# Performance work log

Measured on AMD Instinct MI355X. Metric: run time of the kernel, lower is better.

Reference implementation:

```python
import jax, jax.numpy as jnp
import numpy as np

N, M, D = 32768, 2048, 32


def setup_inputs() -> dict:
    key = jax.random.key(0)
    k1, k2, k3, k4 = jax.random.split(key, 4)
    inputs = jax.random.normal(k1, (N, D), dtype=jnp.float32)
    # matches torch init: abs(10*randn*0.1 + 0.2)
    gamma = jnp.abs(10.0 * jax.random.normal(k2, (M, D, D), dtype=jnp.float32) * 0.1 + 0.2)
    means = jax.random.normal(k3, (M, D), dtype=jnp.float32)
    weights = jax.random.normal(k4, (M,), dtype=jnp.float32)
    return {"inputs": inputs, "gamma": gamma, "means": means, "weights": weights}


def reference(inputs, gamma, means, weights):
    # cov_m = gamma_m @ gamma_m^T  -> symmetric PSD [M, D, D]
    cov = jnp.einsum('mde,mfe->mdf', gamma, gamma)
    # Quadratic form (x - mu)^T C (x - mu) expanded (C symmetric):
    # x^T C_m x via GEMM on flattened outer products: [N, D*D] @ [D*D, M]
    xx = (inputs[:, :, None] * inputs[:, None, :]).reshape(inputs.shape[0], -1)
    quad_x = xx @ cov.reshape(cov.shape[0], -1).T            # [N, M]
    b = jnp.einsum('mde,me->md', cov, means)                 # C_m mu_m, [M, D]
    cross = inputs @ b.T                                     # x^T C_m mu_m, [N, M]
    const = jnp.einsum('md,md->m', b, means)                 # mu^T C mu, [M]
    D_ij = quad_x - 2.0 * cross + const[None, :]             # [N, M]
    out = jnp.exp(-D_ij) @ weights                           # [N]
    return out[:, None]
```

## Files before the change

### kernel.cpp

```cpp
#include <hip/hip_runtime.h>
#include <math.h>


#define NN 32768
#define MM 2048
#define DDIM 32
#define KSYM 576
#define ROWS 128
#define KSTEPS 18
#define SCREEN 120.0f
#define MCAP 2048
#define FCAP 1000000

typedef __attribute__((ext_vector_type(8))) short short8;
typedef __attribute__((ext_vector_type(4))) float floatx4;

__device__ __forceinline__ unsigned int to_bf16(float f) {
  union { float f; unsigned int u; } x; x.f = f;
  return (x.u + 0x7fffu + ((x.u >> 16) & 1u)) >> 16;
}

struct DFTab { unsigned char d[528]; unsigned char f[528]; };
constexpr DFTab make_df() {
  DFTab t{};
  int s = 0;
  for (int d = 0; d < 32; ++d)
    for (int f = d; f < 32; ++f) {
      t.d[s] = (unsigned char)d; t.f[s] = (unsigned char)f; ++s;
    }
  return t;
}
constexpr DFTab DFT = make_df();

__device__ __forceinline__ float slot_val(const float* v, int s) {
  if (s < 528) return v[DFT.d[s]] * v[DFT.f[s]];
  if (s < 560) return v[s - 528];
  if (s < 562) return 1.f;
  return 0.f;
}

__device__ __forceinline__ void slot_df(int s, int* dd, int* ff) {
  int d = 0, b = 0;
  while (b + (DDIM - d) <= s) { b += DDIM - d; ++d; }
  *dd = d; *ff = d + (s - b);
}

__global__ __launch_bounds__(256) void build_b_kernel(
    const float* __restrict__ gamma, const float* __restrict__ means,
    unsigned short* __restrict__ Bm) {
  __shared__ float G[DDIM][DDIM + 1];
  __shared__ float C[DDIM][DDIM + 1];
  __shared__ float bv[DDIM];
  __shared__ float cc;
  const int m = blockIdx.x;
  const int t = threadIdx.x;
  const float* g = gamma + (size_t)m * DDIM * DDIM;
  for (int l = t; l < DDIM * DDIM; l += 256) G[l >> 5][l & 31] = g[l];
  __syncthreads();
  const float* mu = means + m * DDIM;
  for (int l = t; l < DDIM * DDIM; l += 256) {
    int d = l >> 5, f = l & 31;
    float c = 0.f;
#pragma unroll
    for (int e = 0; e < DDIM; ++e) c += G[d][e] * G[f][e];
    C[d][f] = c;
  }
  __syncthreads();
  if (t < DDIM) {
    float b = 0.f;
#pragma unroll
    for (int f = 0; f < DDIM; ++f) b += C[t][f] * mu[f];
    bv[t] = b;
  }
  __syncthreads();
  if (t == 0) {
    float c = 0.f;
#pragma unroll
    for (int d = 0; d < DDIM; ++d) c += bv[d] * mu[d];
    cc = c;
  }
  __syncthreads();
  unsigned short* brow = Bm + (size_t)m * KSYM;
  for (int s = t; s < KSYM; s += 256) {
    float val;
    if (s < 528) {
      int d, f; slot_df(s, &d, &f);
      val = (d == f) ? C[d][d] : 2.f * C[d][f];
    } else if (s < 560) {
      val = -2.f * bv[s - 528];
    } else if (s == 560) {
      val = cc;
    } else if (s == 561) {
      unsigned int hi = to_bf16(cc);
      union { unsigned int u; float f; } xh; xh.u = hi << 16;
      val = cc - xh.f;
    } else {
      val = 0.f;
    }
    brow[s] = (unsigned short)to_bf16(val);
  }
}

__device__ __noinline__ double survivor_contrib(
    int m, const float* __restrict__ gamma, const float* __restrict__ means,
    const float* __restrict__ weights, const float* __restrict__ xrow) {
  const float* mu = means + m * DDIM;
  float v[DDIM];
#pragma unroll
  for (int d = 0; d < DDIM; ++d) v[d] = xrow[d] - mu[d];
  const float* g = gamma + (size_t)m * DDIM * DDIM;
  float Dex = 0.f;
  for (int e = 0; e < DDIM; ++e) {
    float y = 0.f;
#pragma unroll
    for (int d = 0; d < DDIM; ++d) y += g[d * DDIM + e] * v[d];
    Dex += y * y;
  }
  float e2 = -Dex * 1.44269504088896340736f;
  float kf = floorf(e2);
  float mant = exp2f(e2 - kf);
  return ldexp((double)(weights[m] * mant), (int)kf);
}

__global__ __launch_bounds__(512, 2) void screen_kernel(
    const float* __restrict__ x, const unsigned short* __restrict__ Bm,
    unsigned int* __restrict__ mcnt, unsigned short* __restrict__ mlist,
    unsigned int* __restrict__ flist, unsigned int* __restrict__ fcount) {
  extern __shared__ __align__(16) unsigned short As[];
  const int t = threadIdx.x;
  const int i0 = blockIdx.x * ROWS;
  const int lane = t & 63, w = t >> 6;
  const int lrow = lane & 15, quad = lane >> 4;
  const int rot = blockIdx.x & 31;

  {
    const int r = t >> 2, j = t & 3;
    float v[DDIM];
#pragma unroll
    for (int q = 0; q < 8; ++q)
      *(floatx4*)&v[q * 4] = *(const floatx4*)(x + (size_t)(i0 + r) * DDIM + q * 4);
#pragma unroll
    for (int jj = 0; jj < 4; ++jj) {
      if (j == jj) {
#pragma unroll
        for (int cc = 0; cc < 18; ++cc) {
          const int c = jj * 18 + cc;
          unsigned int uu[4];
#pragma unroll
          for (int q = 0; q < 4; ++q) {
            const int s0 = c * 8 + q * 2;
            uu[q] = to_bf16(slot_val(v, s0)) | (to_bf16(slot_val(v, s0 + 1)) << 16);
          }
          const int cs = (c & ~7) | ((c & 7) ^ (r & 7));
          uint4 o; o.x = uu[0]; o.y = uu[1]; o.z = uu[2]; o.w = uu[3];
          *(uint4*)&As[r * KSYM + cs * 8] = o;
        }
      }
    }
  }
  __syncthreads();

#pragma unroll 1
  for (int g = 0; g < 4; ++g) {
    const int mq = ((g * 8 + w) + rot) & 31;
    const int m0 = mq * 64;
    const unsigned short* bb0 = Bm + (size_t)(m0 +  0 + lrow) * KSYM + quad * 8;
    const unsigned short* bb1 = Bm + (size_t)(m0 + 16 + lrow) * KSYM + quad * 8;
    const unsigned short* bb2 = Bm + (size_t)(m0 + 32 + lrow) * KSYM + quad * 8;
    const unsigned short* bb3 = Bm + (size_t)(m0 + 48 + lrow) * KSYM + quad * 8;

    floatx4 acc[8][4] = {};
#pragma unroll
    for (int kk = 0; kk < KSTEPS; ++kk) {
      short8 bf[4];
      bf[0] = *(const short8*)(bb0 + kk * 32);
      bf[1] = *(const short8*)(bb1 + kk * 32);
      bf[2] = *(const short8*)(bb2 + kk * 32);
      bf[3] = *(const short8*)(bb3 + kk * 32);
      short8 af[8];
#pragma unroll
      for (int ti = 0; ti < 8; ++ti) {
        int rr = ti * 16 + lrow;
        int c = kk * 4 + quad;
        int cs = (c & ~7) | ((c & 7) ^ (rr & 7));
        af[ti] = *(const short8*)&As[rr * KSYM + cs * 8];
      }
#pragma unroll
      for (int ti = 0; ti < 8; ++ti)
#pragma unroll
        for (int mj = 0; mj < 4; ++mj)
          acc[ti][mj] = __builtin_amdgcn_mfma_f32_16x16x32_bf16(
              af[ti], bf[mj], acc[ti][mj], 0, 0, 0);
    }

#pragma unroll
    for (int ti = 0; ti < 8; ++ti)
#pragma unroll
      for (int mj = 0; mj < 4; ++mj)
#pragma unroll
        for (int r = 0; r < 4; ++r) {
          float Dt = acc[ti][mj][r];
          if (Dt < SCREEN) {
            int gi = i0 + ti * 16 + quad * 4 + r;
            int gm = m0 + mj * 16 + lrow;
            unsigned int idx = atomicAdd(&mcnt[gm], 1u);
            if (idx < MCAP) {
              mlist[(size_t)gm * MCAP + idx] = (unsigned short)gi;
            } else {
              unsigned int fi = atomicAdd(fcount, 1u);
              if (fi < FCAP)
                flist[fi] = ((unsigned int)gi << 11) | (unsigned int)gm;
            }
          }
        }
  }
}

__global__ __launch_bounds__(256) void survivor2_kernel(
    const unsigned int* __restrict__ mcnt, const unsigned short* __restrict__ mlist,
    const float* __restrict__ x, const float* __restrict__ gamma,
    const float* __restrict__ means, const float* __restrict__ weights,
    double* __restrict__ acc_out) {
  __shared__ float Gt[DDIM][DDIM + 1];
  __shared__ float mu[DDIM];
  const int m = blockIdx.x;
  const int t = threadIdx.x;
  unsigned int cnt = mcnt[m];
  if (cnt > MCAP) cnt = MCAP;
  if (cnt == 0) return;
  const float* g = gamma + (size_t)m * DDIM * DDIM;
  for (int l = t; l < DDIM * DDIM; l += 256) Gt[l & 31][l >> 5] = g[l];
  if (t < DDIM) mu[t] = means[m * DDIM + t];
  __syncthreads();
  const float wm = weights[m];
  for (unsigned int s = t; s < cnt; s += 256) {
    int gi = mlist[(size_t)m * MCAP + s];
    float v[DDIM];
#pragma unroll
    for (int q = 0; q < 8; ++q) {
      floatx4 xv = *(const floatx4*)(x + (size_t)gi * DDIM + q * 4);
      v[q * 4 + 0] = xv.x - mu[q * 4 + 0];
      v[q * 4 + 1] = xv.y - mu[q * 4 + 1];
      v[q * 4 + 2] = xv.z - mu[q * 4 + 2];
      v[q * 4 + 3] = xv.w - mu[q * 4 + 3];
    }
    float Dex = 0.f;
#pragma unroll
    for (int e = 0; e < DDIM; ++e) {
      float y = 0.f;
#pragma unroll
      for (int d = 0; d < DDIM; ++d) y += Gt[e][d] * v[d];
      Dex += y * y;
    }
    float e2 = -Dex * 1.44269504088896340736f;
    float kf = floorf(e2);
    float mant = exp2f(e2 - kf);
    atomicAdd(&acc_out[gi], ldexp((double)(wm * mant), (int)kf));
  }
}

__global__ __launch_bounds__(256) void survivor_fallback_kernel(
    const unsigned int* __restrict__ flist, const unsigned int* __restrict__ fcount,
    const float* __restrict__ x, const float* __restrict__ gamma,
    const float* __restrict__ means, const float* __restrict__ weights,
    double* __restrict__ acc_out) {
  unsigned int total = *fcount;
  if (total > FCAP) total = FCAP;
  for (unsigned int idx = blockIdx.x * 256 + threadIdx.x; idx < total;
       idx += gridDim.x * 256) {
    unsigned int p = flist[idx];
    int gi = (int)(p >> 11), gm = (int)(p & 2047u);
    double c = survivor_contrib(gm, gamma, means, weights, x + (size_t)gi * DDIM);
    atomicAdd(&acc_out[gi], c);
  }
}

__global__ __launch_bounds__(256) void finalize_kernel(
    const double* __restrict__ acc, float* __restrict__ out) {
  int i = blockIdx.x * 256 + threadIdx.x;
  out[i] = (float)acc[i];
}

extern "C" void kernel_launch(void* const* d_in, const int* in_sizes, int n_in,
                              void* d_out, int out_size, void* d_ws, size_t ws_size,
                              hipStream_t stream) {
  (void)in_sizes; (void)n_in; (void)out_size;
  const float* x       = (const float*)d_in[0];
  const float* gamma   = (const float*)d_in[1];
  const float* means   = (const float*)d_in[2];
  const float* weights = (const float*)d_in[3];

  char* p = (char*)d_ws;
  double* acc          = (double*)p;            p += (size_t)NN * 8;
  unsigned int* fcount = (unsigned int*)p;      p += 16;
  unsigned int* mcnt   = (unsigned int*)p;      p += (size_t)MM * 4;
  unsigned short* mlist= (unsigned short*)p;    p += (size_t)MM * MCAP * 2;
  unsigned int* flist  = (unsigned int*)p;      p += (size_t)FCAP * 4;
  unsigned short* Bm   = (unsigned short*)p;    p += (size_t)MM * KSYM * 2;
  const size_t needed = (size_t)(p - (char*)d_ws);
  const size_t zero_bytes = (size_t)NN * 8 + 16 + (size_t)MM * 4;
  if (ws_size < needed) return;

  (void)hipFuncSetAttribute((const void*)screen_kernel,
                            hipFuncAttributeMaxDynamicSharedMemorySize,
                            ROWS * KSYM * 2);

  hipMemsetAsync(d_ws, 0, zero_bytes, stream);
  hipLaunchKernelGGL(build_b_kernel, dim3(MM), dim3(256), 0, stream, gamma, means, Bm);
  hipLaunchKernelGGL(screen_kernel, dim3(NN / ROWS), dim3(512),
                     ROWS * KSYM * 2, stream,
                     x, Bm, mcnt, mlist, flist, fcount);
  hipLaunchKernelGGL(survivor2_kernel, dim3(MM), dim3(256), 0, stream,
                     mcnt, mlist, x, gamma, means, weights, acc);
  hipLaunchKernelGGL(survivor_fallback_kernel, dim3(256), dim3(256), 0, stream,
                     flist, fcount, x, gamma, means, weights, acc);
  hipLaunchKernelGGL(finalize_kernel, dim3(NN / 256), dim3(256), 0, stream,
                     acc, (float*)d_out);
}
```

Measured before the change: 185.6 us.

## Screen with FP8 scaled MFMA and per-component thresholds, merge fallback kernel

The screening GEMM moves from bf16 16x16x32 MFMA to FP8 16x16x128 scaled MFMA. Each component's coefficient row gets a power-of-two block scale, and the constant term becomes a per-component threshold (SCREEN - c), so K drops from 576 to 640 bytes in 5 steps. The screen margin rises to absorb FP8 error, which may admit more survivors into the exact recomputation. The fallback survivor kernel is folded into the main survivor kernel as extra blocks to save a launch.

```diff
diff --git a/kernel.cpp b/kernel.cpp
--- a/kernel.cpp
+++ b/kernel.cpp
@@ -5,15 +5,16 @@
 #define NN 32768
 #define MM 2048
 #define DDIM 32
-#define KSYM 576
+#define KQ 640
 #define ROWS 128
-#define KSTEPS 18
-#define SCREEN 120.0f
+#define KSTEPS 5
+#define SCREEN 160.0f
 #define MCAP 2048
 #define FCAP 1000000
-
-typedef __attribute__((ext_vector_type(8))) short short8;
+#define FBLK 64
+
 typedef __attribute__((ext_vector_type(4))) float floatx4;
+typedef __attribute__((ext_vector_type(8))) int int8v;
 
 __device__ __forceinline__ unsigned int to_bf16(float f) {
   union { float f; unsigned int u; } x; x.f = f;
@@ -35,7 +36,6 @@
 __device__ __forceinline__ float slot_val(const float* v, int s) {
   if (s < 528) return v[DFT.d[s]] * v[DFT.f[s]];
   if (s < 560) return v[s - 528];
-  if (s < 562) return 1.f;
   return 0.f;
 }
 
@@ -47,11 +47,13 @@
 
 __global__ __launch_bounds__(256) void build_b_kernel(
     const float* __restrict__ gamma, const float* __restrict__ means,
-    unsigned short* __restrict__ Bm) {
+    unsigned char* __restrict__ Bm8, unsigned char* __restrict__ sB,
+    float* __restrict__ th) {
   __shared__ float G[DDIM][DDIM + 1];
   __shared__ float C[DDIM][DDIM + 1];
   __shared__ float bv[DDIM];
   __shared__ float cc;
+  __shared__ float rmax[64];
   const int m = blockIdx.x;
   const int t = threadIdx.x;
   const float* g = gamma + (size_t)m * DDIM * DDIM;
@@ -79,25 +81,56 @@
     for (int d = 0; d < DDIM; ++d) c += bv[d] * mu[d];
     cc = c;
   }
-  __syncthreads();
-  unsigned short* brow = Bm + (size_t)m * KSYM;
-  for (int s = t; s < KSYM; s += 256) {
-    float val;
-    if (s < 528) {
-      int d, f; slot_df(s, &d, &f);
-      val = (d == f) ? C[d][d] : 2.f * C[d][f];
-    } else if (s < 560) {
-      val = -2.f * bv[s - 528];
-    } else if (s == 560) {
-      val = cc;
-    } else if (s == 561) {
-      unsigned int hi = to_bf16(cc);
-      union { unsigned int u; float f; } xh; xh.u = hi << 16;
-      val = cc - xh.f;
-    } else {
-      val = 0.f;
-    }
-    brow[s] = (unsigned short)to_bf16(val);
+  float vals[4];
+  float lmax = 0.f;
+  __syncthreads();
+  if (t < 140) {
+#pragma unroll
+    for (int q = 0; q < 4; ++q) {
+      int s = t * 4 + q;
+      float val;
+      if (s < 528) {
+        int d, f; slot_df(s, &d, &f);
+        val = (d == f) ? C[d][d] : 2.f * C[d][f];
+      } else if (s < 560) {
+        val = -2.f * bv[s - 528];
+      } else {
+        val = 0.f;
+      }
+      vals[q] = val;
+      lmax = fmaxf(lmax, fabsf(val));
+    }
+  }
+  if (t < 64) rmax[t] = 0.f;
+  __syncthreads();
+  if (t < 140) {
+    float wmax = lmax;
+#pragma unroll
+    for (int off = 32; off >= 1; off >>= 1)
+      wmax = fmaxf(wmax, __shfl_down(wmax, off, 64));
+    if ((t & 63) == 0) rmax[t >> 6] = wmax;
+  }
+  __syncthreads();
+  __shared__ float sc_inv;
+  __shared__ int sc_e;
+  if (t == 0) {
+    float rm = fmaxf(fmaxf(rmax[0], rmax[1]), fmaxf(rmax[2], rmax[3]));
+    int e = 0;
+    while (rm > 448.f * (float)(1 << e) && e < 16) ++e;
+    sc_e = e;
+    sc_inv = 1.f / (float)(1 << e);
+    sB[m] = (unsigned char)(127 + e);
+    th[m] = SCREEN - cc;
+  }
+  __syncthreads();
+  if (t < 160) {
+    unsigned int dw = 0;
+    if (t < 140) {
+      float si = sc_inv;
+      int d0 = __builtin_amdgcn_cvt_pk_fp8_f32(vals[0] * si, vals[1] * si, 0, false);
+      dw = (unsigned int)__builtin_amdgcn_cvt_pk_fp8_f32(vals[2] * si, vals[3] * si, d0, true);
+    }
+    *(unsigned int*)(Bm8 + (size_t)m * KQ + t * 4) = dw;
   }
 }
 
@@ -123,10 +156,11 @@
 }
 
 __global__ __launch_bounds__(512, 2) void screen_kernel(
-    const float* __restrict__ x, const unsigned short* __restrict__ Bm,
+    const float* __restrict__ x, const unsigned char* __restrict__ Bm8,
+    const unsigned char* __restrict__ sB, const float* __restrict__ th,
     unsigned int* __restrict__ mcnt, unsigned short* __restrict__ mlist,
     unsigned int* __restrict__ flist, unsigned int* __restrict__ fcount) {
-  extern __shared__ __align__(16) unsigned short As[];
+  extern __shared__ __align__(16) unsigned char As[];
   const int t = threadIdx.x;
   const int i0 = blockIdx.x * ROWS;
   const int lane = t & 63, w = t >> 6;
@@ -143,17 +177,21 @@
     for (int jj = 0; jj < 4; ++jj) {
       if (j == jj) {
 #pragma unroll
-        for (int cc = 0; cc < 18; ++cc) {
-          const int c = jj * 18 + cc;
-          unsigned int uu[4];
+        for (int cc = 0; cc < 10; ++cc) {
+          const int c = jj * 10 + cc;
+          uint4 o;
+          unsigned int dw[4];
 #pragma unroll
           for (int q = 0; q < 4; ++q) {
-            const int s0 = c * 8 + q * 2;
-            uu[q] = to_bf16(slot_val(v, s0)) | (to_bf16(slot_val(v, s0 + 1)) << 16);
+            const int s0 = c * 16 + q * 4;
+            int lo = __builtin_amdgcn_cvt_pk_fp8_f32(
+                slot_val(v, s0 + 0), slot_val(v, s0 + 1), 0, false);
+            dw[q] = (unsigned int)__builtin_amdgcn_cvt_pk_fp8_f32(
+                slot_val(v, s0 + 2), slot_val(v, s0 + 3), lo, true);
           }
+          o.x = dw[0]; o.y = dw[1]; o.z = dw[2]; o.w = dw[3];
           const int cs = (c & ~7) | ((c & 7) ^ (r & 7));
-          uint4 o; o.x = uu[0]; o.y = uu[1]; o.z = uu[2]; o.w = uu[3];
-          *(uint4*)&As[r * KSYM + cs * 8] = o;
+          *(uint4*)&As[(size_t)r * KQ + cs * 16] = o;
         }
       }
     }
@@ -164,45 +202,67 @@
   for (int g = 0; g < 4; ++g) {
     const int mq = ((g * 8 + w) + rot) & 31;
     const int m0 = mq * 64;
-    const unsigned short* bb0 = Bm + (size_t)(m0 +  0 + lrow) * KSYM + quad * 8;
-    const unsigned short* bb1 = Bm + (size_t)(m0 + 16 + lrow) * KSYM + quad * 8;
-    const unsigned short* bb2 = Bm + (size_t)(m0 + 32 + lrow) * KSYM + quad * 8;
-    const unsigned short* bb3 = Bm + (size_t)(m0 + 48 + lrow) * KSYM + quad * 8;
+    const unsigned char* bp0 = Bm8 + (size_t)(m0 +  0 + lrow) * KQ + quad * 32;
+    const unsigned char* bp1 = Bm8 + (size_t)(m0 + 16 + lrow) * KQ + quad * 32;
+    const unsigned char* bp2 = Bm8 + (size_t)(m0 + 32 + lrow) * KQ + quad * 32;
+    const unsigned char* bp3 = Bm8 + (size_t)(m0 + 48 + lrow) * KQ + quad * 32;
+    int sb0 = (int)sB[m0 +  0 + lrow] * 0x01010101;
+    int sb1 = (int)sB[m0 + 16 + lrow] * 0x01010101;
+    int sb2 = (int)sB[m0 + 32 + lrow] * 0x01010101;
+    int sb3 = (int)sB[m0 + 48 + lrow] * 0x01010101;
 
     floatx4 acc[8][4] = {};
 #pragma unroll
     for (int kk = 0; kk < KSTEPS; ++kk) {
-      short8 bf[4];
-      bf[0] = *(const short8*)(bb0 + kk * 32);
-      bf[1] = *(const short8*)(bb1 + kk * 32);
-      bf[2] = *(const short8*)(bb2 + kk * 32);
-      bf[3] = *(const short8*)(bb3 + kk * 32);
-      short8 af[8];
+      int8v bf[4];
+#pragma unroll
+      for (int ct = 0; ct < 4; ++ct) {
+        const unsigned char* bp = (ct == 0) ? bp0 : (ct == 1) ? bp1
+                                 : (ct == 2) ? bp2 : bp3;
+        uint4 lo = *(const uint4*)(bp + kk * 128);
+        uint4 hi = *(const uint4*)(bp + kk * 128 + 16);
+        bf[ct][0] = lo.x; bf[ct][1] = lo.y; bf[ct][2] = lo.z; bf[ct][3] = lo.w;
+        bf[ct][4] = hi.x; bf[ct][5] = hi.y; bf[ct][6] = hi.z; bf[ct][7] = hi.w;
+      }
 #pragma unroll
       for (int ti = 0; ti < 8; ++ti) {
-        int rr = ti * 16 + lrow;
-        int c = kk * 4 + quad;
-        int cs = (c & ~7) | ((c & 7) ^ (rr & 7));
-        af[ti] = *(const short8*)&As[rr * KSYM + cs * 8];
-      }
-#pragma unroll
-      for (int ti = 0; ti < 8; ++ti)
-#pragma unroll
-        for (int mj = 0; mj < 4; ++mj)
-          acc[ti][mj] = __builtin_amdgcn_mfma_f32_16x16x32_bf16(
-              af[ti], bf[mj], acc[ti][mj], 0, 0, 0);
-    }
-
+        const int rr = ti * 16 + lrow;
+        const int c0 = kk * 8 + quad * 2;
+        const int cs0 = (c0 & ~7) | ((c0 & 7) ^ (rr & 7));
+        const int c1 = c0 + 1;
+        const int cs1 = (c1 & ~7) | ((c1 & 7) ^ (rr & 7));
+        uint4 lo = *(const uint4*)&As[(size_t)rr * KQ + cs0 * 16];
+        uint4 hi = *(const uint4*)&As[(size_t)rr * KQ + cs1 * 16];
+        int8v af;
+        af[0] = lo.x; af[1] = lo.y; af[2] = lo.z; af[3] = lo.w;
+        af[4] = hi.x; af[5] = hi.y; af[6] = hi.z; af[7] = hi.w;
+        acc[ti][0] = __builtin_amdgcn_mfma_scale_f32_16x16x128_f8f6f4(
+            af, bf[0], acc[ti][0], 0, 0, 0, 0x7F7F7F7F, 0, sb0);
+        acc[ti][1] = __builtin_amdgcn_mfma_scale_f32_16x16x128_f8f6f4(
+            af, bf[1], acc[ti][1], 0, 0, 0, 0x7F7F7F7F, 0, sb1);
+        acc[ti][2] = __builtin_amdgcn_mfma_scale_f32_16x16x128_f8f6f4(
+            af, bf[2], acc[ti][2], 0, 0, 0, 0x7F7F7F7F, 0, sb2);
+        acc[ti][3] = __builtin_amdgcn_mfma_scale_f32_16x16x128_f8f6f4(
+            af, bf[3], acc[ti][3], 0, 0, 0, 0x7F7F7F7F, 0, sb3);
+      }
+    }
+
+    const float th0 = th[m0 +  0 + lrow];
+    const float th1 = th[m0 + 16 + lrow];
+    const float th2 = th[m0 + 32 + lrow];
+    const float th3 = th[m0 + 48 + lrow];
 #pragma unroll
     for (int ti = 0; ti < 8; ++ti)
 #pragma unroll
-      for (int mj = 0; mj < 4; ++mj)
+      for (int ct = 0; ct < 4; ++ct) {
+        const float tht = (ct == 0) ? th0 : (ct == 1) ? th1
+                          : (ct == 2) ? th2 : th3;
 #pragma unroll
         for (int r = 0; r < 4; ++r) {
-          float Dt = acc[ti][mj][r];
-          if (Dt < SCREEN) {
+          float Dt = acc[ti][ct][r];
+          if (Dt < tht) {
             int gi = i0 + ti * 16 + quad * 4 + r;
-            int gm = m0 + mj * 16 + lrow;
+            int gm = m0 + ct * 16 + lrow;
             unsigned int idx = atomicAdd(&mcnt[gm], 1u);
             if (idx < MCAP) {
               mlist[(size_t)gm * MCAP + idx] = (unsigned short)gi;
@@ -213,18 +273,32 @@
             }
           }
         }
+      }
   }
 }
 
 __global__ __launch_bounds__(256) void survivor2_kernel(
     const unsigned int* __restrict__ mcnt, const unsigned short* __restrict__ mlist,
+    const unsigned int* __restrict__ flist, const unsigned int* __restrict__ fcount,
     const float* __restrict__ x, const float* __restrict__ gamma,
     const float* __restrict__ means, const float* __restrict__ weights,
     double* __restrict__ acc_out) {
+  const int blk = blockIdx.x;
+  const int t = threadIdx.x;
+  if (blk >= MM) {
+    unsigned int total = *fcount;
+    if (total > FCAP) total = FCAP;
+    for (unsigned int idx = (blk - MM) * 256 + t; idx < total; idx += FBLK * 256) {
+      unsigned int p = flist[idx];
+      int gi = (int)(p >> 11), gm = (int)(p & 2047u);
+      double c = survivor_contrib(gm, gamma, means, weights, x + (size_t)gi * DDIM);
+      atomicAdd(&acc_out[gi], c);
+    }
+    return;
+  }
   __shared__ float Gt[DDIM][DDIM + 1];
   __shared__ float mu[DDIM];
-  const int m = blockIdx.x;
-  const int t = threadIdx.x;
+  const int m = blk;
   unsigned int cnt = mcnt[m];
   if (cnt > MCAP) cnt = MCAP;
   if (cnt == 0) return;
@@ -256,22 +330,6 @@
     float kf = floorf(e2);
     float mant = exp2f(e2 - kf);
     atomicAdd(&acc_out[gi], ldexp((double)(wm * mant), (int)kf));
-  }
-}
-
-__global__ __launch_bounds__(256) void survivor_fallback_kernel(
-    const unsigned int* __restrict__ flist, const unsigned int* __restrict__ fcount,
-    const float* __restrict__ x, const float* __restrict__ gamma,
-    const float* __restrict__ means, const float* __restrict__ weights,
-    double* __restrict__ acc_out) {
-  unsigned int total = *fcount;
-  if (total > FCAP) total = FCAP;
-  for (unsigned int idx = blockIdx.x * 256 + threadIdx.x; idx < total;
-       idx += gridDim.x * 256) {
-    unsigned int p = flist[idx];
-    int gi = (int)(p >> 11), gm = (int)(p & 2047u);
-    double c = survivor_contrib(gm, gamma, means, weights, x + (size_t)gi * DDIM);
-    atomicAdd(&acc_out[gi], c);
   }
 }
 
@@ -296,24 +354,26 @@
   unsigned int* mcnt   = (unsigned int*)p;      p += (size_t)MM * 4;
   unsigned short* mlist= (unsigned short*)p;    p += (size_t)MM * MCAP * 2;
   unsigned int* flist  = (unsigned int*)p;      p += (size_t)FCAP * 4;
-  unsigned short* Bm   = (unsigned short*)p;    p += (size_t)MM * KSYM * 2;
+  unsigned char* Bm8   = (unsigned char*)p;     p += (size_t)MM * KQ;
+  unsigned char* sB    = (unsigned char*)p;     p += (size_t)MM;
+  p = (char*)(((uintptr_t)p + 15) & ~(uintptr_t)15);
+  float* th            = (float*)p;             p += (size_t)MM * 4;
   const size_t needed = (size_t)(p - (char*)d_ws);
   const size_t zero_bytes = (size_t)NN * 8 + 16 + (size_t)MM * 4;
   if (ws_size < needed) return;
 
   (void)hipFuncSetAttribute((const void*)screen_kernel,
                             hipFuncAttributeMaxDynamicSharedMemorySize,
-                            ROWS * KSYM * 2);
+                            ROWS * KQ);
 
   hipMemsetAsync(d_ws, 0, zero_bytes, stream);
-  hipLaunchKernelGGL(build_b_kernel, dim3(MM), dim3(256), 0, stream, gamma, means, Bm);
+  hipLaunchKernelGGL(build_b_kernel, dim3(MM), dim3(256), 0, stream,
+                     gamma, means, Bm8, sB, th);
   hipLaunchKernelGGL(screen_kernel, dim3(NN / ROWS), dim3(512),
-                     ROWS * KSYM * 2, stream,
-                     x, Bm, mcnt, mlist, flist, fcount);
-  hipLaunchKernelGGL(survivor2_kernel, dim3(MM), dim3(256), 0, stream,
-                     mcnt, mlist, x, gamma, means, weights, acc);
-  hipLaunchKernelGGL(survivor_fallback_kernel, dim3(256), dim3(256), 0, stream,
-                     flist, fcount, x, gamma, means, weights, acc);
+                     ROWS * KQ, stream,
+                     x, Bm8, sB, th, mcnt, mlist, flist, fcount);
+  hipLaunchKernelGGL(survivor2_kernel, dim3(MM + FBLK), dim3(256), 0, stream,
+                     mcnt, mlist, flist, fcount, x, gamma, means, weights, acc);
   hipLaunchKernelGGL(finalize_kernel, dim3(NN / 256), dim3(256), 0, stream,
                      acc, (float*)d_out);
 }
```

Result: slower. 593.5 us (+219.8%).
